# Kernel optimization log

Measured on AMD Instinct MI355X. Metric: run time of the kernel, lower is better.

## Reference

```python
import jax, jax.numpy as jnp
import numpy as np

MP = 10242  # number of coarse (pooled) vertices = L.shape[0]


def setup_inputs() -> dict:
    key = jax.random.key(0)
    k1, k2, k3, k4 = jax.random.split(key, 4)
    B, M, F = 16, 40962, 128
    NNZ = 40968  # ~4 nonzeros per coarse vertex (barycentric pooling)
    x = jax.random.normal(k1, (B, M, F), dtype=jnp.float32)
    rows = jax.random.randint(k2, (NNZ,), 0, MP, dtype=jnp.int64)
    cols = jax.random.randint(k3, (NNZ,), 0, M, dtype=jnp.int64)
    vals = jax.random.uniform(k4, (NNZ,), dtype=jnp.float32)
    return {"x": x, "rows": rows, "cols": cols, "vals": vals}


def reference(x, rows, cols, vals):
    # Equivalent of tf.sparse_tensor_dense_matmul(L, reshape(transpose(x)))
    # L: sparse [Mp, M] in COO (rows, cols, vals); x: [B, M, F].
    # out[b, p, f] = sum_{k: rows[k]==p} vals[k] * x[b, cols[k], f]
    gathered = x[:, cols, :] * vals[None, :, None]          # [B, nnz, F]
    gathered = jnp.transpose(gathered, (1, 0, 2))           # [nnz, B, F]
    pooled = jax.ops.segment_sum(gathered, rows, num_segments=MP)  # [Mp, B, F]
    return jnp.transpose(pooled, (1, 0, 2))                 # [B, Mp, F]
```

## Files before the change

kernel.cpp:

```cpp
#include <hip/hip_runtime.h>
#include <hip/hip_bf16.h>

constexpr int MP = 10242;
constexpr int B  = 16;
constexpr int M  = 40962;
constexpr int F  = 128;
constexpr int SCAN_THREADS = 1024;
constexpr int SCAN_ITEMS = (MP + SCAN_THREADS - 1) / SCAN_THREADS;

__global__ void hist_kernel(const int* __restrict__ rows,
                            int* __restrict__ counts, int nnz) {
    int k = blockIdx.x * blockDim.x + threadIdx.x;
    if (k < nnz) atomicAdd(&counts[rows[k]], 1);
}

__global__ __launch_bounds__(SCAN_THREADS)
void scan_kernel(const int* __restrict__ counts,
                 int* __restrict__ offsets,
                 int* __restrict__ cursor) {
    __shared__ int lds[SCAN_THREADS];
    int t = threadIdx.x;
    int local[SCAN_ITEMS];
    int run = 0;
    int base_idx = t * SCAN_ITEMS;
    for (int i = 0; i < SCAN_ITEMS; ++i) {
        int idx = base_idx + i;
        int c = (idx < MP) ? counts[idx] : 0;
        local[i] = run;
        run += c;
    }
    lds[t] = run;
    __syncthreads();
    for (int off = 1; off < SCAN_THREADS; off <<= 1) {
        int v = (t >= off) ? lds[t - off] : 0;
        __syncthreads();
        lds[t] += v;
        __syncthreads();
    }
    int excl = lds[t] - run;
    for (int i = 0; i < SCAN_ITEMS; ++i) {
        int idx = base_idx + i;
        if (idx < MP) {
            int o = excl + local[i];
            offsets[idx] = o;
            cursor[idx]  = o;
        }
    }
    if (t == SCAN_THREADS - 1) offsets[MP] = lds[SCAN_THREADS - 1];
}

__global__ void scatter_kernel(const int* __restrict__ rows,
                               const int* __restrict__ cols,
                               const float* __restrict__ vals,
                               int* __restrict__ cursor,
                               int* __restrict__ scol,
                               float* __restrict__ sval, int nnz) {
    int k = blockIdx.x * blockDim.x + threadIdx.x;
    if (k < nnz) {
        int p = rows[k];
        int pos = atomicAdd(&cursor[p], 1);
        scol[pos] = cols[k];
        sval[pos] = vals[k];
    }
}

__global__ __launch_bounds__(256)
void pool_kernel(const float* __restrict__ x,
                 const int* __restrict__ offsets,
                 const int* __restrict__ scol,
                 const float* __restrict__ sval,
                 float* __restrict__ out) {
    int w    = blockIdx.x * 4 + (threadIdx.x >> 6);
    int lane = threadIdx.x & 63;
    int p = w >> 4;
    int b = w & 15;
    int s = offsets[p];
    int e = offsets[p + 1];
    const float2* xb = (const float2*)x + (size_t)b * (size_t)M * (F / 2);
    float2 acc; acc.x = 0.f; acc.y = 0.f;
    for (int i = s; i < e; ++i) {
        int col = scol[i];
        float v = sval[i];
        float2 xv = xb[(size_t)col * (F / 2) + lane];
        acc.x = fmaf(v, xv.x, acc.x);
        acc.y = fmaf(v, xv.y, acc.y);
    }
    ((float2*)out)[((size_t)b * MP + p) * (F / 2) + lane] = acc;
}

extern "C" void kernel_launch(void* const* d_in, const int* in_sizes, int n_in,
                              void* d_out, int out_size, void* d_ws, size_t ws_size,
                              hipStream_t stream) {
    const float* x    = (const float*)d_in[0];
    const int*   rows = (const int*)d_in[1];
    const int*   cols = (const int*)d_in[2];
    const float* vals = (const float*)d_in[3];
    float* out = (float*)d_out;
    const int nnz = in_sizes[1];

    int* counts  = (int*)d_ws;
    int* offsets = counts + MP;
    int* cursor  = offsets + (MP + 1);
    int* scol    = cursor + MP;
    float* sval  = (float*)(scol + nnz);

    hipMemsetAsync(counts, 0, MP * sizeof(int), stream);

    int nb = (nnz + 255) / 256;
    hist_kernel<<<nb, 256, 0, stream>>>(rows, counts, nnz);
    scan_kernel<<<1, SCAN_THREADS, 0, stream>>>(counts, offsets, cursor);
    scatter_kernel<<<nb, 256, 0, stream>>>(rows, cols, vals, cursor, scol, sval, nnz);

    int pool_blocks = (MP * B) / 4;
    pool_kernel<<<pool_blocks, 256, 0, stream>>>(x, offsets, scol, sval, out);
}
```

Baseline: 518.8 us.

## Fuse CSR build into one LDS kernel and vectorize pooling gather

```diff
diff --git a/kernel.cpp b/kernel.cpp
--- a/kernel.cpp
+++ b/kernel.cpp
@@ -5,87 +5,104 @@
 constexpr int B  = 16;
 constexpr int M  = 40962;
 constexpr int F  = 128;
-constexpr int SCAN_THREADS = 1024;
-constexpr int SCAN_ITEMS = (MP + SCAN_THREADS - 1) / SCAN_THREADS;
+constexpr int ST = 1024;
+constexpr int ITEMS = (MP + ST - 1) / ST;
 
-__global__ void hist_kernel(const int* __restrict__ rows,
-                            int* __restrict__ counts, int nnz) {
-    int k = blockIdx.x * blockDim.x + threadIdx.x;
-    if (k < nnz) atomicAdd(&counts[rows[k]], 1);
-}
+__global__ __launch_bounds__(ST)
+void setup_kernel(const int* __restrict__ rows,
+                  const int* __restrict__ cols,
+                  const float* __restrict__ vals,
+                  int* __restrict__ offsets,
+                  int* __restrict__ scol,
+                  float* __restrict__ sval,
+                  int nnz) {
+    __shared__ int cnt[MP];
+    __shared__ int wsum[ST];
+    int t = threadIdx.x;
 
-__global__ __launch_bounds__(SCAN_THREADS)
-void scan_kernel(const int* __restrict__ counts,
-                 int* __restrict__ offsets,
-                 int* __restrict__ cursor) {
-    __shared__ int lds[SCAN_THREADS];
-    int t = threadIdx.x;
-    int local[SCAN_ITEMS];
+    for (int i = t; i < MP; i += ST) cnt[i] = 0;
+    __syncthreads();
+
+    for (int k = t; k < nnz; k += ST) atomicAdd(&cnt[rows[k]], 1);
+    __syncthreads();
+
+    int base = t * ITEMS;
+    int local[ITEMS];
     int run = 0;
-    int base_idx = t * SCAN_ITEMS;
-    for (int i = 0; i < SCAN_ITEMS; ++i) {
-        int idx = base_idx + i;
-        int c = (idx < MP) ? counts[idx] : 0;
+    for (int i = 0; i < ITEMS; ++i) {
+        int idx = base + i;
+        int c = (idx < MP) ? cnt[idx] : 0;
         local[i] = run;
         run += c;
     }
-    lds[t] = run;
+    wsum[t] = run;
     __syncthreads();
-    for (int off = 1; off < SCAN_THREADS; off <<= 1) {
-        int v = (t >= off) ? lds[t - off] : 0;
+    for (int off = 1; off < ST; off <<= 1) {
+        int v = (t >= off) ? wsum[t - off] : 0;
         __syncthreads();
-        lds[t] += v;
+        wsum[t] += v;
         __syncthreads();
     }
-    int excl = lds[t] - run;
-    for (int i = 0; i < SCAN_ITEMS; ++i) {
-        int idx = base_idx + i;
+    int excl = wsum[t] - run;
+    for (int i = 0; i < ITEMS; ++i) {
+        int idx = base + i;
         if (idx < MP) {
             int o = excl + local[i];
+            cnt[idx] = o;
             offsets[idx] = o;
-            cursor[idx]  = o;
         }
     }
-    if (t == SCAN_THREADS - 1) offsets[MP] = lds[SCAN_THREADS - 1];
-}
+    if (t == ST - 1) offsets[MP] = wsum[ST - 1];
+    __syncthreads();
 
-__global__ void scatter_kernel(const int* __restrict__ rows,
-                               const int* __restrict__ cols,
-                               const float* __restrict__ vals,
-                               int* __restrict__ cursor,
-                               int* __restrict__ scol,
-                               float* __restrict__ sval, int nnz) {
-    int k = blockIdx.x * blockDim.x + threadIdx.x;
-    if (k < nnz) {
+    for (int k = t; k < nnz; k += ST) {
         int p = rows[k];
-        int pos = atomicAdd(&cursor[p], 1);
+        int pos = atomicAdd(&cnt[p], 1);
         scol[pos] = cols[k];
         sval[pos] = vals[k];
     }
 }
 
 __global__ __launch_bounds__(256)
-void pool_kernel(const float* __restrict__ x,
+void pool_kernel(const float4* __restrict__ x,
                  const int* __restrict__ offsets,
                  const int* __restrict__ scol,
                  const float* __restrict__ sval,
-                 float* __restrict__ out) {
+                 float4* __restrict__ out) {
     int w    = blockIdx.x * 4 + (threadIdx.x >> 6);
     int lane = threadIdx.x & 63;
-    int p = w >> 4;
-    int b = w & 15;
+    int p = w >> 3;
+    int b = ((w & 7) << 1) | (lane >> 5);
+    int l = lane & 31;
+
     int s = offsets[p];
     int e = offsets[p + 1];
-    const float2* xb = (const float2*)x + (size_t)b * (size_t)M * (F / 2);
-    float2 acc; acc.x = 0.f; acc.y = 0.f;
-    for (int i = s; i < e; ++i) {
-        int col = scol[i];
+    const float4* xb = x + (size_t)b * M * (F / 4);
+
+    float4 acc; acc.x = acc.y = acc.z = acc.w = 0.f;
+    int i = s;
+    for (; i + 4 <= e; i += 4) {
+        int   c0 = scol[i],     c1 = scol[i + 1], c2 = scol[i + 2], c3 = scol[i + 3];
+        float v0 = sval[i],     v1 = sval[i + 1], v2 = sval[i + 2], v3 = sval[i + 3];
+        float4 a0 = xb[(size_t)c0 * (F / 4) + l];
+        float4 a1 = xb[(size_t)c1 * (F / 4) + l];
+        float4 a2 = xb[(size_t)c2 * (F / 4) + l];
+        float4 a3 = xb[(size_t)c3 * (F / 4) + l];
+        acc.x = fmaf(v0, a0.x, fmaf(v1, a1.x, fmaf(v2, a2.x, fmaf(v3, a3.x, acc.x))));
+        acc.y = fmaf(v0, a0.y, fmaf(v1, a1.y, fmaf(v2, a2.y, fmaf(v3, a3.y, acc.y))));
+        acc.z = fmaf(v0, a0.z, fmaf(v1, a1.z, fmaf(v2, a2.z, fmaf(v3, a3.z, acc.z))));
+        acc.w = fmaf(v0, a0.w, fmaf(v1, a1.w, fmaf(v2, a2.w, fmaf(v3, a3.w, acc.w))));
+    }
+    for (; i < e; ++i) {
+        int c = scol[i];
         float v = sval[i];
-        float2 xv = xb[(size_t)col * (F / 2) + lane];
-        acc.x = fmaf(v, xv.x, acc.x);
-        acc.y = fmaf(v, xv.y, acc.y);
+        float4 a = xb[(size_t)c * (F / 4) + l];
+        acc.x = fmaf(v, a.x, acc.x);
+        acc.y = fmaf(v, a.y, acc.y);
+        acc.z = fmaf(v, a.z, acc.z);
+        acc.w = fmaf(v, a.w, acc.w);
     }
-    ((float2*)out)[((size_t)b * MP + p) * (F / 2) + lane] = acc;
+    out[((size_t)b * MP + p) * (F / 4) + l] = acc;
 }
 
 extern "C" void kernel_launch(void* const* d_in, const int* in_sizes, int n_in,
@@ -98,19 +115,12 @@
     float* out = (float*)d_out;
     const int nnz = in_sizes[1];
 
-    int* counts  = (int*)d_ws;
-    int* offsets = counts + MP;
-    int* cursor  = offsets + (MP + 1);
-    int* scol    = cursor + MP;
-    float* sval  = (float*)(scol + nnz);
+    int*   offsets = (int*)d_ws;
+    int*   scol    = offsets + (MP + 1);
+    float* sval    = (float*)(scol + nnz);
 
-    hipMemsetAsync(counts, 0, MP * sizeof(int), stream);
+    setup_kernel<<<1, ST, 0, stream>>>(rows, cols, vals, offsets, scol, sval, nnz);
 
-    int nb = (nnz + 255) / 256;
-    hist_kernel<<<nb, 256, 0, stream>>>(rows, counts, nnz);
-    scan_kernel<<<1, SCAN_THREADS, 0, stream>>>(counts, offsets, cursor);
-    scatter_kernel<<<nb, 256, 0, stream>>>(rows, cols, vals, cursor, scol, sval, nnz);
-
-    int pool_blocks = (MP * B) / 4;
-    pool_kernel<<<pool_blocks, 256, 0, stream>>>(x, offsets, scol, sval, out);
+    pool_kernel<<<MP * 2, 256, 0, stream>>>((const float4*)x, offsets, scol, sval,
+                                            (float4*)out);
 }
```

Result: slower. 578.3 us (+11.5%).
